# Optimization experiments

Measured on AMD Instinct MI355X. Metric: run time of the kernel, lower is better.

The kernel has to match this reference:

```python
import jax, jax.numpy as jnp
import numpy as np

B, S, D_IN, D_H = 16, 4096, 512, 512

def setup_inputs() -> dict:
    key = jax.random.key(0)
    ks = jax.random.split(key, 8)
    inp = {
        "input": jax.random.normal(ks[0], (B, D_IN), dtype=jnp.float32),
        "context": jax.random.normal(ks[1], (B, S, D_IN), dtype=jnp.float32),
        "mask": jax.random.bernoulli(ks[2], 0.2, (B, S)),
        # parameters (torch nn.Linear layout: W [out,in], b [out])
        "W_in": jax.random.normal(ks[3], (D_H, D_IN), dtype=jnp.float32) / np.sqrt(D_IN),
        "b_in": jax.random.normal(ks[4], (D_H,), dtype=jnp.float32) * 0.01,
        "W_ctx": jax.random.normal(ks[5], (D_H, D_IN), dtype=jnp.float32) / np.sqrt(D_IN),
        "b_ctx": jax.random.normal(ks[6], (D_H,), dtype=jnp.float32) * 0.01,
        "v": jax.random.normal(ks[7], (D_H,), dtype=jnp.float32),
    }
    return inp


def reference(input, context, mask, W_in, b_in, W_ctx, b_ctx, v):
    # inp: [B, H] projected decoder state
    inp = input @ W_in.T + b_in
    # ctx: [B, S, H] projected context (this is what the torch code matmuls
    # with the softmax weights, i.e. hidden lives in hidden_dim space)
    ctx = context @ W_ctx.T + b_ctx
    # additive (Bahdanau) scores: v . tanh(inp + ctx) -> [B, S]
    scores = jnp.einsum("h,bsh->bs", v, jnp.tanh(inp[:, None, :] + ctx))
    # masked positions get -inf so they receive zero softmax weight
    scores = jnp.where(mask, -jnp.inf, scores)
    attn = jax.nn.softmax(scores, axis=-1)  # [B, S]
    # weighted sum of projected context: [B, H]
    hidden = jnp.einsum("bsh,bs->bh", ctx, attn)
    return hidden, attn
```

## Files before the change

kernel.cpp:

```cpp
#include <hip/hip_runtime.h>
#include <hip/hip_bf16.h>

#define B_  16
#define S_  4096
#define DIN 512
#define DH  512

typedef _Float16 f16x8 __attribute__((ext_vector_type(8)));
typedef float    f32x4 __attribute__((ext_vector_type(4)));


__device__ __forceinline__ float fast_tanh(float x) {
    float e = __expf(2.f * x);
    return 1.f - 2.f * __builtin_amdgcn_rcpf(e + 1.f);
}

__device__ __forceinline__ void gload_lds16(const void* g, void* l) {
    __builtin_amdgcn_global_load_lds(
        (const __attribute__((address_space(1))) void*)g,
        (__attribute__((address_space(3))) void*)l, 16, 0, 0);
}

__device__ __forceinline__ int mask_at(const void* mask, int isByte, int idx) {
    return isByte ? (int)((const unsigned char*)mask)[idx]
                  : ((const int*)mask)[idx];
}

__global__ __launch_bounds__(256)
void prep_kernel(const float* __restrict__ input,
                 const float* __restrict__ W_in,
                 const float* __restrict__ b_in,
                 const float* __restrict__ context,
                 const float* __restrict__ W_ctx,
                 const float* __restrict__ b_ctx,
                 const void*  __restrict__ mask,
                 _Float16* __restrict__ W16,
                 _Float16* __restrict__ ctx16,
                 float* __restrict__ addv,
                 float* __restrict__ zeroRegion,
                 int* __restrict__ maskflag) {
    int blk = blockIdx.x;
    int tid = threadIdx.x;
    if (blk < 8192) {
#pragma unroll
        for (int it = 0; it < 4; ++it) {
            int base = blk * 4096 + it * 1024 + tid * 4;
            float4 wv = *(const float4*)(context + base);
            union { _Float16 f[4]; ushort4 u; } cv;
            cv.f[0] = (_Float16)wv.x; cv.f[1] = (_Float16)wv.y;
            cv.f[2] = (_Float16)wv.z; cv.f[3] = (_Float16)wv.w;
            *(ushort4*)(ctx16 + base) = cv.u;
        }
    } else if (blk < 8448) {
        int base = (blk - 8192) * 1024 + tid * 4;
        float4 wv = *(const float4*)(W_ctx + base);
        union { _Float16 f[4]; ushort4 u; } cv;
        cv.f[0] = (_Float16)wv.x; cv.f[1] = (_Float16)wv.y;
        cv.f[2] = (_Float16)wv.z; cv.f[3] = (_Float16)wv.w;
        *(ushort4*)(W16 + base) = cv.u;
    } else if (blk < 8480) {
        int t = blk - 8448;
        int b = t >> 1;
        int h = ((t & 1) << 8) + tid;
        __shared__ float inrow[DIN];
        inrow[tid]       = input[b * DIN + tid];
        inrow[tid + 256] = input[b * DIN + tid + 256];
        __syncthreads();
        const float* wr = W_in + (size_t)h * DIN;
        float acc = 0.f;
        for (int k = 0; k < DIN; k += 4) {
            float4 w4 = *(const float4*)(wr + k);
            acc += w4.x * inrow[k] + w4.y * inrow[k + 1]
                 + w4.z * inrow[k + 2] + w4.w * inrow[k + 3];
        }
        addv[b * DH + h] = acc + b_in[h] + b_ctx[h];
    } else if (blk == 8480) {
        const uint4* m4 = (const uint4*)mask;
        unsigned int orw = 0;
#pragma unroll
        for (int it = 0; it < 16; ++it) {
            uint4 w = m4[it * 256 + tid];
            orw |= (w.x | w.y | w.z | w.w);
        }
        int found = ((orw & 0xFFFFFF00u) != 0) ? 1 : 0;
        __shared__ int f;
        if (tid == 0) f = 0;
        __syncthreads();
        if (found) atomicOr(&f, 1);
        __syncthreads();
        if (tid == 0) maskflag[0] = f;
    } else {
        int base = (blk - 8481) * 4096;
#pragma unroll
        for (int it = 0; it < 16; ++it)
            zeroRegion[base + it * 256 + tid] = 0.f;
    }
}

__global__ __launch_bounds__(256)
void score_kernel(const _Float16* __restrict__ ctx16,
                  const _Float16* __restrict__ W16,
                  const float* __restrict__ addv,
                  const float* __restrict__ v,
                  float* __restrict__ scores) {
    __shared__ __align__(16) _Float16 As[2][4096];
    __shared__ __align__(16) _Float16 Bs[2][4096];

    const int tid  = threadIdx.x;
    const int wave = tid >> 6;
    const int lane = tid & 63;
    const int l15  = lane & 15;
    const int q    = lane >> 4;
    const int sg   = wave >> 1;
    const int ng   = wave & 1;

    const int xcd  = blockIdx.x & 7;
    const int slot = blockIdx.x >> 3;
    const int nt   = slot & 3;
    const int g    = (slot >> 2) * 8 + xcd;
    const int b    = g >> 5;
    const int st   = g & 31;
    const int s0   = st * 128;
    const int n0   = nt * 128;

    const _Float16* ctxA = ctx16 + ((size_t)b * S_ + s0) * DIN;

#define STAGE(kc_, buf_)                                                       \
    {                                                                          \
        _Pragma("unroll")                                                      \
        for (int u = 0; u < 4; ++u) {                                          \
            int id = wave * 4 + u;                                             \
            if (id < 8) {                                                      \
                const _Float16* gp = ctxA +                                    \
                    (size_t)(id * 16 + l15) * DIN + (kc_) * 32 + q * 8;        \
                gload_lds16(gp, &As[buf_][id * 512]);                          \
            } else {                                                           \
                int jn = id - 8;                                               \
                const _Float16* gp = W16 +                                     \
                    (size_t)(n0 + jn * 16 + l15) * DIN + (kc_) * 32 + q * 8;   \
                gload_lds16(gp, &Bs[buf_][jn * 512]);                          \
            }                                                                  \
        }                                                                      \
    }

    f32x4 acc[4][4];
#pragma unroll
    for (int jm = 0; jm < 4; ++jm)
#pragma unroll
        for (int jn = 0; jn < 4; ++jn) acc[jm][jn] = (f32x4){0.f, 0.f, 0.f, 0.f};

    STAGE(0, 0);

    for (int kc = 0; kc < 16; ++kc) {
        __syncthreads();
        int buf = kc & 1;
        if (kc + 1 < 16) STAGE(kc + 1, buf ^ 1);

        f16x8 afr[4], bfr[4];
#pragma unroll
        for (int jm = 0; jm < 4; ++jm)
            afr[jm] = *(const f16x8*)&As[buf][(sg * 4 + jm) * 512 + q * 128 + l15 * 8];
#pragma unroll
        for (int jn = 0; jn < 4; ++jn)
            bfr[jn] = *(const f16x8*)&Bs[buf][(ng * 4 + jn) * 512 + q * 128 + l15 * 8];

#pragma unroll
        for (int jn = 0; jn < 4; ++jn)
#pragma unroll
            for (int jm = 0; jm < 4; ++jm)
                acc[jm][jn] = __builtin_amdgcn_mfma_f32_16x16x32_f16(
                    afr[jm], bfr[jn], acc[jm][jn], 0, 0, 0);
    }

    const float* avb = addv + b * DH;
    float rowsum[4][4] = {{0.f,0.f,0.f,0.f},{0.f,0.f,0.f,0.f},
                          {0.f,0.f,0.f,0.f},{0.f,0.f,0.f,0.f}};
#pragma unroll
    for (int jn = 0; jn < 4; ++jn) {
        int n = n0 + (ng * 4 + jn) * 16 + l15;
        float av = avb[n];
        float vv = v[n];
#pragma unroll
        for (int jm = 0; jm < 4; ++jm)
#pragma unroll
            for (int r = 0; r < 4; ++r)
                rowsum[jm][r] += vv * fast_tanh(acc[jm][jn][r] + av);
    }
#pragma unroll
    for (int jm = 0; jm < 4; ++jm)
#pragma unroll
        for (int r = 0; r < 4; ++r) {
            float s = rowsum[jm][r];
            s += __shfl_xor(s, 1, 16);
            s += __shfl_xor(s, 2, 16);
            s += __shfl_xor(s, 4, 16);
            s += __shfl_xor(s, 8, 16);
            if (l15 == 0) {
                int srow = s0 + (sg * 4 + jm) * 16 + q * 4 + r;
                atomicAdd(&scores[b * S_ + srow], s);
            }
        }
}

__global__ __launch_bounds__(256)
void attnwsum_kernel(const float* __restrict__ scores,
                     const float* __restrict__ context,
                     const void* __restrict__ mask,
                     const int* __restrict__ maskflag,
                     float* __restrict__ attn,
                     float* __restrict__ wsum) {
    __shared__ float rbuf[8];
    __shared__ int   selIdx[64];
    __shared__ float selW[64];
    __shared__ int   selCount;

    int b  = blockIdx.x >> 6;
    int c0 = (blockIdx.x & 63) * 64;
    int tid = threadIdx.x;
    int wv = tid >> 6, ln = tid & 63;
    int isByte = maskflag[0];
    const float* sr = scores + b * S_;

    float mx = -__builtin_inff();
    float vals[16];
#pragma unroll
    for (int it = 0; it < 16; ++it) {
        int s = it * 256 + tid;
        float x = mask_at(mask, isByte, b * S_ + s) ? -__builtin_inff() : sr[s];
        vals[it] = x;
        mx = fmaxf(mx, x);
    }
    for (int o = 1; o < 64; o <<= 1) mx = fmaxf(mx, __shfl_xor(mx, o, 64));
    if (ln == 0) rbuf[wv] = mx;
    __syncthreads();
    mx = fmaxf(fmaxf(rbuf[0], rbuf[1]), fmaxf(rbuf[2], rbuf[3]));

    float sum = 0.f;
#pragma unroll
    for (int it = 0; it < 16; ++it) sum += __expf(vals[it] - mx);
    for (int o = 1; o < 64; o <<= 1) sum += __shfl_xor(sum, o, 64);
    if (ln == 0) rbuf[4 + wv] = sum;
    if (tid == 0) selCount = 0;
    __syncthreads();
    float inv = 1.f / (rbuf[4] + rbuf[5] + rbuf[6] + rbuf[7]);

    if (tid < 64) {
        int s = c0 + tid;
        int idx = b * S_ + s;
        float sc = mask_at(mask, isByte, idx) ? -__builtin_inff() : sr[s];
        float p = __expf(sc - mx) * inv;
        attn[idx] = p;
        if (p > 1e-9f) {
            int k = atomicAdd(&selCount, 1);
            selIdx[k] = s;
            selW[k]  = p;
        }
    }
    __syncthreads();

    int cnt = selCount;
    if (cnt == 0) return;
    const float* cb = context + (size_t)b * S_ * DIN;
    float a00 = 0.f, a01 = 0.f, a10 = 0.f, a11 = 0.f;
    float a20 = 0.f, a21 = 0.f, a30 = 0.f, a31 = 0.f;
    int i = 0;
    for (; i + 4 <= cnt; i += 4) {
        const float* c0p = cb + (size_t)selIdx[i]     * DIN;
        const float* c1p = cb + (size_t)selIdx[i + 1] * DIN;
        const float* c2p = cb + (size_t)selIdx[i + 2] * DIN;
        const float* c3p = cb + (size_t)selIdx[i + 3] * DIN;
        float w0 = selW[i], w1 = selW[i + 1], w2 = selW[i + 2], w3 = selW[i + 3];
        a00 += w0 * c0p[tid]; a01 += w0 * c0p[tid + 256];
        a10 += w1 * c1p[tid]; a11 += w1 * c1p[tid + 256];
        a20 += w2 * c2p[tid]; a21 += w2 * c2p[tid + 256];
        a30 += w3 * c3p[tid]; a31 += w3 * c3p[tid + 256];
    }
    float acc0 = (a00 + a10) + (a20 + a30);
    float acc1 = (a01 + a11) + (a21 + a31);
    for (; i < cnt; ++i) {
        const float* cr = cb + (size_t)selIdx[i] * DIN;
        float w = selW[i];
        acc0 += w * cr[tid];
        acc1 += w * cr[tid + 256];
    }
    atomicAdd(&wsum[b * DIN + tid], acc0);
    atomicAdd(&wsum[b * DIN + tid + 256], acc1);
}

__global__ __launch_bounds__(256)
void hidden_kernel(const float* __restrict__ W_ctx,
                   const float* __restrict__ b_ctx,
                   const float* __restrict__ wsum,
                   float* __restrict__ hidden) {
    int b = blockIdx.x >> 1;
    int tid = threadIdx.x;
    int h = ((blockIdx.x & 1) << 8) + tid;
    __shared__ float wrow[DIN];
    wrow[tid]       = wsum[b * DIN + tid];
    wrow[tid + 256] = wsum[b * DIN + tid + 256];
    __syncthreads();
    const float* wr = W_ctx + (size_t)h * DIN;
    float acc = 0.f;
    for (int k = 0; k < DIN; k += 4) {
        float4 w4 = *(const float4*)(wr + k);
        acc += w4.x * wrow[k] + w4.y * wrow[k + 1]
             + w4.z * wrow[k + 2] + w4.w * wrow[k + 3];
    }
    hidden[b * DH + h] = acc + b_ctx[h];
}

extern "C" void kernel_launch(void* const* d_in, const int* in_sizes, int n_in,
                              void* d_out, int out_size, void* d_ws, size_t ws_size,
                              hipStream_t stream) {
    const float* input   = (const float*)d_in[0];
    const float* context = (const float*)d_in[1];
    const void*  mask    = d_in[2];
    const float* W_in    = (const float*)d_in[3];
    const float* b_in    = (const float*)d_in[4];
    const float* W_ctx   = (const float*)d_in[5];
    const float* b_ctx   = (const float*)d_in[6];
    const float* v       = (const float*)d_in[7];

    char* ws = (char*)d_ws;
    _Float16* W16   = (_Float16*)ws;
    _Float16* ctx16 = (_Float16*)(ws + 524288);
    float* addv     = (float*)(ws + 67633152);
    float* scores   = (float*)(ws + 67665920);
    float* wsum     = (float*)(ws + 67928064);
    int*   maskflag = (int*)(ws + 67960832);

    float* hidden = (float*)d_out;
    float* attn   = (float*)d_out + B_ * DH;

    prep_kernel<<<8547, 256, 0, stream>>>(input, W_in, b_in, context, W_ctx,
                                          b_ctx, mask, W16, ctx16, addv,
                                          scores , maskflag);
    score_kernel<<<2048, 256, 0, stream>>>(ctx16, W16, addv, v, scores);
    attnwsum_kernel<<<B_ * 64, 256, 0, stream>>>(scores, context, mask, maskflag,
                                                 attn, wsum);
    hidden_kernel<<<B_ * 2, 256, 0, stream>>>(W_ctx, b_ctx, wsum, hidden);
}
```

Baseline: 323.0 us.

## Fuse fp32-to-fp16 context conversion into score GEMM and widen N tile

Removes the separate pass that converted the full context tensor to fp16 in a workspace buffer. The score kernel now loads fp32 context rows straight into registers, converts them, and writes fp16 tiles to LDS, with register double-buffering two K-steps ahead. The N tile is widened from 128 to 256, which halves the grid and means each context tile is read by two blocks instead of four. This saves one full write and re-read of a 64 MB intermediate, at the cost of more registers (32 accumulators per thread), larger LDS use, and conversion work inside the GEMM loop.

```diff
diff --git a/kernel.cpp b/kernel.cpp
--- a/kernel.cpp
+++ b/kernel.cpp
@@ -30,36 +30,24 @@
 void prep_kernel(const float* __restrict__ input,
                  const float* __restrict__ W_in,
                  const float* __restrict__ b_in,
-                 const float* __restrict__ context,
                  const float* __restrict__ W_ctx,
                  const float* __restrict__ b_ctx,
                  const void*  __restrict__ mask,
                  _Float16* __restrict__ W16,
-                 _Float16* __restrict__ ctx16,
                  float* __restrict__ addv,
                  float* __restrict__ zeroRegion,
                  int* __restrict__ maskflag) {
     int blk = blockIdx.x;
     int tid = threadIdx.x;
-    if (blk < 8192) {
-#pragma unroll
-        for (int it = 0; it < 4; ++it) {
-            int base = blk * 4096 + it * 1024 + tid * 4;
-            float4 wv = *(const float4*)(context + base);
-            union { _Float16 f[4]; ushort4 u; } cv;
-            cv.f[0] = (_Float16)wv.x; cv.f[1] = (_Float16)wv.y;
-            cv.f[2] = (_Float16)wv.z; cv.f[3] = (_Float16)wv.w;
-            *(ushort4*)(ctx16 + base) = cv.u;
-        }
-    } else if (blk < 8448) {
-        int base = (blk - 8192) * 1024 + tid * 4;
+    if (blk < 256) {
+        int base = blk * 1024 + tid * 4;
         float4 wv = *(const float4*)(W_ctx + base);
         union { _Float16 f[4]; ushort4 u; } cv;
         cv.f[0] = (_Float16)wv.x; cv.f[1] = (_Float16)wv.y;
         cv.f[2] = (_Float16)wv.z; cv.f[3] = (_Float16)wv.w;
         *(ushort4*)(W16 + base) = cv.u;
-    } else if (blk < 8480) {
-        int t = blk - 8448;
+    } else if (blk < 288) {
+        int t = blk - 256;
         int b = t >> 1;
         int h = ((t & 1) << 8) + tid;
         __shared__ float inrow[DIN];
@@ -74,7 +62,7 @@
                  + w4.z * inrow[k + 2] + w4.w * inrow[k + 3];
         }
         addv[b * DH + h] = acc + b_in[h] + b_ctx[h];
-    } else if (blk == 8480) {
+    } else if (blk == 288) {
         const uint4* m4 = (const uint4*)mask;
         unsigned int orw = 0;
 #pragma unroll
@@ -90,7 +78,7 @@
         __syncthreads();
         if (tid == 0) maskflag[0] = f;
     } else {
-        int base = (blk - 8481) * 4096;
+        int base = (blk - 289) * 4096;
 #pragma unroll
         for (int it = 0; it < 16; ++it)
             zeroRegion[base + it * 256 + tid] = 0.f;
@@ -98,13 +86,13 @@
 }
 
 __global__ __launch_bounds__(256)
-void score_kernel(const _Float16* __restrict__ ctx16,
+void score_kernel(const float* __restrict__ context,
                   const _Float16* __restrict__ W16,
                   const float* __restrict__ addv,
                   const float* __restrict__ v,
                   float* __restrict__ scores) {
     __shared__ __align__(16) _Float16 As[2][4096];
-    __shared__ __align__(16) _Float16 Bs[2][4096];
+    __shared__ __align__(16) _Float16 Bs[2][8192];
 
     const int tid  = threadIdx.x;
     const int wave = tid >> 6;
@@ -116,68 +104,102 @@
 
     const int xcd  = blockIdx.x & 7;
     const int slot = blockIdx.x >> 3;
-    const int nt   = slot & 3;
-    const int g    = (slot >> 2) * 8 + xcd;
+    const int nt   = slot & 1;
+    const int g    = (slot >> 1) * 8 + xcd;
     const int b    = g >> 5;
     const int st   = g & 31;
     const int s0   = st * 128;
-    const int n0   = nt * 128;
-
-    const _Float16* ctxA = ctx16 + ((size_t)b * S_ + s0) * DIN;
-
-#define STAGE(kc_, buf_)                                                       \
+    const int n0   = nt * 256;
+
+    const float* ctxA = context + ((size_t)b * S_ + s0) * DIN;
+
+    const int rowA0 = ((tid >> 6) * 16) + (tid & 15);
+    const int kbA0  = ((tid >> 4) & 3) * 8;
+    const int rowA1 = rowA0 + 64;
+    const int kbA1  = kbA0;
+
+#define STAGE_B(kc_, buf_)                                                     \
     {                                                                          \
         _Pragma("unroll")                                                      \
         for (int u = 0; u < 4; ++u) {                                          \
-            int id = wave * 4 + u;                                             \
-            if (id < 8) {                                                      \
-                const _Float16* gp = ctxA +                                    \
-                    (size_t)(id * 16 + l15) * DIN + (kc_) * 32 + q * 8;        \
-                gload_lds16(gp, &As[buf_][id * 512]);                          \
-            } else {                                                           \
-                int jn = id - 8;                                               \
-                const _Float16* gp = W16 +                                     \
-                    (size_t)(n0 + jn * 16 + l15) * DIN + (kc_) * 32 + q * 8;   \
-                gload_lds16(gp, &Bs[buf_][jn * 512]);                          \
-            }                                                                  \
+            int jn = wave * 4 + u;                                             \
+            const _Float16* gp = W16 +                                         \
+                (size_t)(n0 + jn * 16 + l15) * DIN + (kc_) * 32 + q * 8;       \
+            gload_lds16(gp, &Bs[buf_][jn * 512]);                              \
         }                                                                      \
     }
 
-    f32x4 acc[4][4];
+#define LOADA(kc_, set_)                                                       \
+    {                                                                          \
+        const float* g0 = ctxA + (size_t)rowA0 * DIN + (kc_) * 32 + kbA0;      \
+        const float* g1 = ctxA + (size_t)rowA1 * DIN + (kc_) * 32 + kbA1;      \
+        set_[0] = *(const float4*)g0; set_[1] = *(const float4*)(g0 + 4);      \
+        set_[2] = *(const float4*)g1; set_[3] = *(const float4*)(g1 + 4);      \
+    }
+
+#define WRITEA(set_, buf_)                                                     \
+    {                                                                          \
+        f16x8 h0, h1;                                                          \
+        h0[0] = (_Float16)set_[0].x; h0[1] = (_Float16)set_[0].y;              \
+        h0[2] = (_Float16)set_[0].z; h0[3] = (_Float16)set_[0].w;              \
+        h0[4] = (_Float16)set_[1].x; h0[5] = (_Float16)set_[1].y;              \
+        h0[6] = (_Float16)set_[1].z; h0[7] = (_Float16)set_[1].w;              \
+        h1[0] = (_Float16)set_[2].x; h1[1] = (_Float16)set_[2].y;              \
+        h1[2] = (_Float16)set_[2].z; h1[3] = (_Float16)set_[2].w;              \
+        h1[4] = (_Float16)set_[3].x; h1[5] = (_Float16)set_[3].y;              \
+        h1[6] = (_Float16)set_[3].z; h1[7] = (_Float16)set_[3].w;              \
+        *(f16x8*)&As[buf_][tid * 8]        = h0;                               \
+        *(f16x8*)&As[buf_][tid * 8 + 2048] = h1;                               \
+    }
+
+    f32x4 acc[4][8];
 #pragma unroll
     for (int jm = 0; jm < 4; ++jm)
 #pragma unroll
-        for (int jn = 0; jn < 4; ++jn) acc[jm][jn] = (f32x4){0.f, 0.f, 0.f, 0.f};
-
-    STAGE(0, 0);
-
-    for (int kc = 0; kc < 16; ++kc) {
-        __syncthreads();
-        int buf = kc & 1;
-        if (kc + 1 < 16) STAGE(kc + 1, buf ^ 1);
-
-        f16x8 afr[4], bfr[4];
-#pragma unroll
-        for (int jm = 0; jm < 4; ++jm)
-            afr[jm] = *(const f16x8*)&As[buf][(sg * 4 + jm) * 512 + q * 128 + l15 * 8];
-#pragma unroll
-        for (int jn = 0; jn < 4; ++jn)
-            bfr[jn] = *(const f16x8*)&Bs[buf][(ng * 4 + jn) * 512 + q * 128 + l15 * 8];
-
-#pragma unroll
-        for (int jn = 0; jn < 4; ++jn)
-#pragma unroll
-            for (int jm = 0; jm < 4; ++jm)
-                acc[jm][jn] = __builtin_amdgcn_mfma_f32_16x16x32_f16(
-                    afr[jm], bfr[jn], acc[jm][jn], 0, 0, 0);
+        for (int jn = 0; jn < 8; ++jn) acc[jm][jn] = (f32x4){0.f, 0.f, 0.f, 0.f};
+
+    float4 aA[4], aB[4];
+
+    STAGE_B(0, 0);
+    LOADA(0, aA);
+    WRITEA(aA, 0);
+    LOADA(1, aB);
+    __syncthreads();
+
+#define STEP(kc_, buf_, ldset_, wrset_)                                        \
+    {                                                                          \
+        f16x8 afr[4], bfr[8];                                                  \
+        _Pragma("unroll")                                                      \
+        for (int jm = 0; jm < 4; ++jm)                                         \
+            afr[jm] = *(const f16x8*)&As[buf_][(sg * 4 + jm) * 512 +           \
+                                              q * 128 + l15 * 8];              \
+        _Pragma("unroll")                                                      \
+        for (int jn = 0; jn < 8; ++jn)                                         \
+            bfr[jn] = *(const f16x8*)&Bs[buf_][(ng * 8 + jn) * 512 +           \
+                                              q * 128 + l15 * 8];              \
+        if ((kc_) + 2 < 16) LOADA((kc_) + 2, ldset_);                          \
+        if ((kc_) + 1 < 16) STAGE_B((kc_) + 1, (buf_) ^ 1);                    \
+        _Pragma("unroll")                                                      \
+        for (int jn = 0; jn < 8; ++jn)                                         \
+            _Pragma("unroll")                                                  \
+            for (int jm = 0; jm < 4; ++jm)                                     \
+                acc[jm][jn] = __builtin_amdgcn_mfma_f32_16x16x32_f16(          \
+                    afr[jm], bfr[jn], acc[jm][jn], 0, 0, 0);                   \
+        if ((kc_) + 1 < 16) WRITEA(wrset_, (buf_) ^ 1);                        \
+        __syncthreads();                                                       \
+    }
+
+    for (int kp = 0; kp < 8; ++kp) {
+        STEP(2 * kp,     0, aA, aB);
+        STEP(2 * kp + 1, 1, aB, aA);
     }
 
     const float* avb = addv + b * DH;
     float rowsum[4][4] = {{0.f,0.f,0.f,0.f},{0.f,0.f,0.f,0.f},
                           {0.f,0.f,0.f,0.f},{0.f,0.f,0.f,0.f}};
 #pragma unroll
-    for (int jn = 0; jn < 4; ++jn) {
-        int n = n0 + (ng * 4 + jn) * 16 + l15;
+    for (int jn = 0; jn < 8; ++jn) {
+        int n = n0 + (ng * 8 + jn) * 16 + l15;
         float av = avb[n];
         float vv = v[n];
 #pragma unroll
@@ -323,19 +345,18 @@
 
     char* ws = (char*)d_ws;
     _Float16* W16   = (_Float16*)ws;
-    _Float16* ctx16 = (_Float16*)(ws + 524288);
-    float* addv     = (float*)(ws + 67633152);
-    float* scores   = (float*)(ws + 67665920);
-    float* wsum     = (float*)(ws + 67928064);
-    int*   maskflag = (int*)(ws + 67960832);
+    float* addv     = (float*)(ws + 524288);
+    float* scores   = (float*)(ws + 557056);
+    float* wsum     = (float*)(ws + 819200);
+    int*   maskflag = (int*)(ws + 851968);
 
     float* hidden = (float*)d_out;
     float* attn   = (float*)d_out + B_ * DH;
 
-    prep_kernel<<<8547, 256, 0, stream>>>(input, W_in, b_in, context, W_ctx,
-                                          b_ctx, mask, W16, ctx16, addv,
-                                          scores , maskflag);
-    score_kernel<<<2048, 256, 0, stream>>>(ctx16, W16, addv, v, scores);
+    prep_kernel<<<307, 256, 0, stream>>>(input, W_in, b_in, W_ctx, b_ctx, mask,
+                                         W16, addv, scores ,
+                                         maskflag);
+    score_kernel<<<1024, 256, 0, stream>>>(context, W16, addv, v, scores);
     attnwsum_kernel<<<B_ * 64, 256, 0, stream>>>(scores, context, mask, maskflag,
                                                  attn, wsum);
     hidden_kernel<<<B_ * 2, 256, 0, stream>>>(W_ctx, b_ctx, wsum, hidden);
```

Result: slower. 343.6 us (+6.4%).
